# Performance work log

Hardware: AMD Instinct MI355X
Metric: run time of the kernel (lower is better)

## Reference

```python
import jax, jax.numpy as jnp
import numpy as np

N_NODES = 100000
N_EDGES = 1600000
IN_CH = 128
HID = 128
BN_EPS = 1e-5


def setup_inputs() -> dict:
    key = jax.random.key(0)
    ks = jax.random.split(key, 16)
    x = jax.random.normal(ks[0], (N_NODES, IN_CH), dtype=jnp.float32)
    edge_index = jax.random.randint(ks[1], (2, N_EDGES), 0, N_NODES, dtype=jnp.int32)
    edge_attr = jax.random.uniform(ks[2], (N_EDGES,), dtype=jnp.float32)
    def glorot(k, fan_in, fan_out):
        s = jnp.sqrt(6.0 / (fan_in + fan_out))
        return jax.random.uniform(k, (fan_in, fan_out), dtype=jnp.float32, minval=-s, maxval=s)
    W1 = glorot(ks[3], IN_CH, HID)
    b1 = jnp.zeros((HID,), jnp.float32)
    gamma1 = jnp.ones((HID,), jnp.float32)
    beta1 = jnp.zeros((HID,), jnp.float32)
    W2 = glorot(ks[4], HID, HID)
    b2 = jnp.zeros((HID,), jnp.float32)
    gamma2 = jnp.ones((HID,), jnp.float32)
    beta2 = jnp.zeros((HID,), jnp.float32)
    W3 = glorot(ks[5], HID, 1)
    b3 = jnp.zeros((1,), jnp.float32)
    return {"x": x, "edge_index": edge_index, "edge_attr": edge_attr,
            "W1": W1, "b1": b1, "gamma1": gamma1, "beta1": beta1,
            "W2": W2, "b2": b2, "gamma2": gamma2, "beta2": beta2,
            "W3": W3, "b3": b3}


def _gcn_norm(edge_index, edge_weight, num_nodes):
    # PyG gcn_norm with add_self_loops=True, self-loop weight 1.0
    sl = jnp.arange(num_nodes, dtype=edge_index.dtype)
    row = jnp.concatenate([edge_index[0], sl])  # source
    col = jnp.concatenate([edge_index[1], sl])  # target
    w = jnp.concatenate([edge_weight, jnp.ones((num_nodes,), edge_weight.dtype)])
    deg = jax.ops.segment_sum(w, col, num_segments=num_nodes)
    dinv = jnp.where(deg > 0, jax.lax.rsqrt(jnp.maximum(deg, 1e-30)), 0.0)
    norm = dinv[row] * w * dinv[col]
    return row, col, norm


def _gcn_conv(x, W, b, row, col, norm, num_nodes):
    xw = x @ W                       # [N, out]
    msg = xw[row] * norm[:, None]    # gather + scale, [E+N, out]
    out = jax.ops.segment_sum(msg, col, num_segments=num_nodes)  # scatter-add
    return out + b


def _batchnorm(x, gamma, beta):
    mean = jnp.mean(x, axis=0)
    var = jnp.mean(jnp.square(x - mean), axis=0)  # biased var (torch BN)
    return (x - mean) * jax.lax.rsqrt(var + BN_EPS) * gamma + beta


def reference(x, edge_index, edge_attr, W1, b1, gamma1, beta1, W2, b2, gamma2, beta2, W3, b3):
    n = x.shape[0]
    row, col, norm = _gcn_norm(edge_index, edge_attr, n)
    h = _gcn_conv(x, W1, b1, row, col, norm, n)
    h = jax.nn.relu(_batchnorm(h, gamma1, beta1))  # dropout = identity (eval)
    h = _gcn_conv(h, W2, b2, row, col, norm, n)
    h = jax.nn.relu(_batchnorm(h, gamma2, beta2))
    out = _gcn_conv(h, W3, b3, row, col, norm, n)  # [N, 1]
    return out
```

## Files before the change

kernel.cpp:

```cpp
#include <hip/hip_runtime.h>
#include <hip/hip_bf16.h>


#define HID 128
#define BN_EPS 1e-5f
#define BK 48
#define NPB 128
#define NBMAX 1024
#define CH_A 6144
#define BINCAP 2432

typedef __attribute__((ext_vector_type(8))) short bf16x8;
typedef __attribute__((ext_vector_type(4))) float f32x4;

static inline size_t alignup(size_t x){ return (x + 255) & ~(size_t)255; }


static __device__ inline float2 bf16pair(unsigned int u){
  __hip_bfloat162 h = *(__hip_bfloat162*)&u;
  return __bfloat1622float2(h);
}

static __device__ inline unsigned int packpair(float x, float y){
  __hip_bfloat162 p = __float22bfloat162_rn({x, y});
  return *(unsigned int*)&p;
}

static __device__ inline uint2 pack_bf16x4(float4 a){
  uint2 r;
  r.x = packpair(a.x, a.y);
  r.y = packpair(a.z, a.w);
  return r;
}

static __device__ inline unsigned short bfbits(float v){
  __hip_bfloat16 h = __float2bfloat16(v);
  return *(unsigned short*)&h;
}

__global__ void k_wtprep2(const float* __restrict__ W1, const float* __restrict__ W2,
                          unsigned short* __restrict__ wt1, unsigned short* __restrict__ wt2){
  int idx = blockIdx.x*256 + threadIdx.x;
  const float* Wg = (idx < 16384) ? W1 : W2;
  unsigned short* WTg = (idx < 16384) ? wt1 : wt2;
  int i = idx & 16383;
  int k   = i >> 7;
  int col = i & 127;
  WTg[(size_t)col*128 + k] = bfbits(Wg[(size_t)k*128 + col]);
}


__global__ __launch_bounds__(256) void k_partA(const int* __restrict__ ei,
    const float* __restrict__ attr, int* __restrict__ binCur,
    int2* __restrict__ binbuf, int E){
  __shared__ int hist[NBMAX];
  __shared__ int pref[NBMAX];
  __shared__ int gbase[NBMAX];
  __shared__ int tmp[256];
  __shared__ int2 stage[CH_A];
  __shared__ unsigned short sbin[CH_A];
  int e0 = blockIdx.x * CH_A;
  for (int b = threadIdx.x; b < NBMAX; b += 256) hist[b] = 0;
  __syncthreads();
  #pragma unroll
  for (int k = 0; k < CH_A/256; ++k){
    int e = e0 + k*256 + threadIdx.x;
    if (e < E) atomicAdd(&hist[ei[E + e] >> 7], 1);
  }
  __syncthreads();
  int b4 = threadIdx.x * 4;
  int h0 = hist[b4], h1 = hist[b4+1], h2 = hist[b4+2], h3 = hist[b4+3];
  int lsum = h0 + h1 + h2 + h3;
  tmp[threadIdx.x] = lsum;
  __syncthreads();
  #pragma unroll
  for (int d = 1; d < 256; d <<= 1){
    int t = (threadIdx.x >= d) ? tmp[threadIdx.x - d] : 0;
    __syncthreads();
    tmp[threadIdx.x] += t;
    __syncthreads();
  }
  int ex = tmp[threadIdx.x] - lsum;
  pref[b4]   = ex;
  pref[b4+1] = ex + h0;
  pref[b4+2] = ex + h0 + h1;
  pref[b4+3] = ex + h0 + h1 + h2;
  gbase[b4]   = h0 ? atomicAdd(&binCur[b4],   h0) : 0;
  gbase[b4+1] = h1 ? atomicAdd(&binCur[b4+1], h1) : 0;
  gbase[b4+2] = h2 ? atomicAdd(&binCur[b4+2], h2) : 0;
  gbase[b4+3] = h3 ? atomicAdd(&binCur[b4+3], h3) : 0;
  hist[b4] = pref[b4]; hist[b4+1] = pref[b4+1];
  hist[b4+2] = pref[b4+2]; hist[b4+3] = pref[b4+3];
  __syncthreads();
  #pragma unroll
  for (int k = 0; k < CH_A/256; ++k){
    int e = e0 + k*256 + threadIdx.x;
    if (e < E){
      int d = ei[E + e];
      int s = ei[e];
      int bin = d >> 7;
      int p = atomicAdd(&hist[bin], 1);
      stage[p] = make_int2(s | ((d & 127) << 17), __float_as_int(attr[e]));
      sbin[p] = (unsigned short)bin;
    }
  }
  __syncthreads();
  int cnt = (e0 + CH_A <= E) ? CH_A : max(E - e0, 0);
  for (int i = threadIdx.x; i < cnt; i += 256){
    int bin = sbin[i];
    int off = gbase[bin] + (i - pref[bin]);
    if (off < BINCAP)
      binbuf[(size_t)bin*BINCAP + off] = stage[i];
  }
}

__global__ __launch_bounds__(256) void k_partB(const int2* __restrict__ binbuf,
    const int* __restrict__ binCur, int2* __restrict__ csr,
    int* __restrict__ cnt, float* __restrict__ dinv, int N){
  __shared__ int2 lb[NPB*BK];
  __shared__ int lcnt[NPB];
  int bin = blockIdx.x;
  int node0 = bin * NPB;
  for (int i = threadIdx.x; i < NPB; i += 256) lcnt[i] = 0;
  __syncthreads();
  int m = min(binCur[bin], BINCAP);
  for (int i = threadIdx.x; i < m; i += 256){
    int2 rec = binbuf[(size_t)bin*BINCAP + i];
    int dlo = (rec.x >> 17) & 127;
    int s   = rec.x & 0x1FFFF;
    int p = atomicAdd(&lcnt[dlo], 1);
    if (p < BK) lb[dlo*BK + p] = make_int2(s, rec.y);
  }
  __syncthreads();
  if (threadIdx.x < NPB){
    int node = node0 + threadIdx.x;
    if (node < N){
      int c = min(lcnt[threadIdx.x], BK);
      float s = 0.f;
      for (int k = 0; k < c; ++k) s += __int_as_float(lb[threadIdx.x*BK + k].y);
      cnt[node] = c;
      dinv[node] = 1.0f / sqrtf(1.0f + s);
    }
  }
  int lim = min(NPB, N - node0) * BK;
  for (int i = threadIdx.x; i < lim; i += 256)
    csr[(size_t)node0*BK + i] = lb[i];
}

template<bool BN, bool AB16>
__device__ inline void gemm_body(const void* __restrict__ Av,
    const unsigned short* __restrict__ WTg, const float* __restrict__ coef,
    const float* __restrict__ dinv,
    unsigned int* __restrict__ C, int n, int bid){
  int lane = threadIdx.x & 63;
  int wv4  = threadIdx.x >> 6;
  int l16  = lane & 15;
  int kg   = lane >> 4;
  int row_base = bid*128 + wv4*32;
  int nm1 = n - 1;
  int a0row = min(row_base + l16,      nm1);
  int a1row = min(row_base + 16 + l16, nm1);

  f32x4 acc[2][8] = {};
  #pragma unroll
  for (int k0 = 0; k0 < 128; k0 += 32){
    int k = k0 + kg*8;
    float4 sca, scb, sha, shb;
    if (BN){
      sca = *(const float4*)(coef + k);
      scb = *(const float4*)(coef + k + 4);
      sha = *(const float4*)(coef + 128 + k);
      shb = *(const float4*)(coef + 128 + k + 4);
    }
    bf16x8 a0, a1;
    if constexpr (AB16){
      const unsigned int* A = (const unsigned int*)Av;
      uint4 u0 = *(const uint4*)(A + (size_t)a0row*64 + (k >> 1));
      uint4 u1 = *(const uint4*)(A + (size_t)a1row*64 + (k >> 1));
      #pragma unroll
      for (int half = 0; half < 2; ++half){
        uint4 u = half ? u1 : u0;
        float2 p0 = bf16pair(u.x), p1 = bf16pair(u.y);
        float2 p2 = bf16pair(u.z), p3 = bf16pair(u.w);
        if (BN){
          p0.x = fmaxf(fmaf(p0.x, sca.x, sha.x), 0.f);
          p0.y = fmaxf(fmaf(p0.y, sca.y, sha.y), 0.f);
          p1.x = fmaxf(fmaf(p1.x, sca.z, sha.z), 0.f);
          p1.y = fmaxf(fmaf(p1.y, sca.w, sha.w), 0.f);
          p2.x = fmaxf(fmaf(p2.x, scb.x, shb.x), 0.f);
          p2.y = fmaxf(fmaf(p2.y, scb.y, shb.y), 0.f);
          p3.x = fmaxf(fmaf(p3.x, scb.z, shb.z), 0.f);
          p3.y = fmaxf(fmaf(p3.y, scb.w, shb.w), 0.f);
        }
        union { bf16x8 v; unsigned int u[4]; } c;
        c.u[0] = packpair(p0.x, p0.y);
        c.u[1] = packpair(p1.x, p1.y);
        c.u[2] = packpair(p2.x, p2.y);
        c.u[3] = packpair(p3.x, p3.y);
        if (half) a1 = c.v; else a0 = c.v;
      }
    } else {
      const float* A = (const float*)Av;
      float4 lo0 = *(const float4*)(A + (size_t)a0row*HID + k);
      float4 hi0 = *(const float4*)(A + (size_t)a0row*HID + k + 4);
      float4 lo1 = *(const float4*)(A + (size_t)a1row*HID + k);
      float4 hi1 = *(const float4*)(A + (size_t)a1row*HID + k + 4);
      union { bf16x8 v; uint2 u[2]; } a0c, a1c;
      a0c.u[0] = pack_bf16x4(lo0); a0c.u[1] = pack_bf16x4(hi0);
      a1c.u[0] = pack_bf16x4(lo1); a1c.u[1] = pack_bf16x4(hi1);
      a0 = a0c.v; a1 = a1c.v;
    }
    #pragma unroll
    for (int ct = 0; ct < 8; ++ct){
      int col = ct*16 + l16;
      bf16x8 b = *(const bf16x8*)(WTg + (size_t)col*128 + k);
      acc[0][ct] = __builtin_amdgcn_mfma_f32_16x16x32_bf16(a0, b, acc[0][ct], 0,0,0);
      acc[1][ct] = __builtin_amdgcn_mfma_f32_16x16x32_bf16(a1, b, acc[1][ct], 0,0,0);
    }
  }

  #pragma unroll
  for (int rt = 0; rt < 2; ++rt){
    int growb = row_base + rt*16 + kg*4;
    #pragma unroll
    for (int r = 0; r < 4; ++r){
      int grow = growb + r;
      bool ok = (grow < n) && !(lane & 1);
      float dv = ok ? dinv[grow] : 0.f;
      #pragma unroll
      for (int ct = 0; ct < 8; ++ct){
        float v = acc[rt][ct][r];
        float o = __shfl_xor(v, 1);
        if (ok)
          C[(size_t)grow*64 + ct*8 + (l16 >> 1)] = packpair(v*dv, o*dv);
      }
    }
  }
}

__global__ __launch_bounds__(256) void k_gemm_mfma_s(const float* __restrict__ A,
    const unsigned short* __restrict__ WTg, const float* __restrict__ dinv,
    unsigned int* __restrict__ C, int n){
  gemm_body<false,false>(A, WTg, nullptr, dinv, C, n, blockIdx.x);
}

__global__ __launch_bounds__(256) void k_gemm_mfma_bn16_s(const unsigned int* __restrict__ A,
    const unsigned short* __restrict__ WTg, const float* __restrict__ coef,
    const float* __restrict__ dinv, unsigned int* __restrict__ C, int n){
  gemm_body<true,true>(A, WTg, coef, dinv, C, n, blockIdx.x);
}


struct Acc8 { float a0,a1,a2,a3,a4,a5,a6,a7; };

static __device__ inline void fma8(Acc8& a, uint4 v, float wt){
  float2 p0 = bf16pair(v.x), p1 = bf16pair(v.y);
  float2 p2 = bf16pair(v.z), p3 = bf16pair(v.w);
  a.a0 = fmaf(wt, p0.x, a.a0); a.a1 = fmaf(wt, p0.y, a.a1);
  a.a2 = fmaf(wt, p1.x, a.a2); a.a3 = fmaf(wt, p1.y, a.a3);
  a.a4 = fmaf(wt, p2.x, a.a4); a.a5 = fmaf(wt, p2.y, a.a5);
  a.a6 = fmaf(wt, p3.x, a.a6); a.a7 = fmaf(wt, p3.y, a.a7);
}

__global__ __launch_bounds__(256) void k_gather128(const unsigned int* __restrict__ yb,
    const int2* __restrict__ csr, const int* __restrict__ cnt,
    const float* __restrict__ dinv, const float* __restrict__ bias,
    unsigned int* __restrict__ out, int n){
  int node = blockIdx.x*4 + (threadIdx.x >> 6);
  int lane = threadIdx.x & 63;
  if (node >= n) return;
  int l16 = lane & 15;
  int eg  = lane >> 4;
  size_t base = (size_t)node*BK;
  int m = min(cnt[node], BK);
  Acc8 a = {0,0,0,0,0,0,0,0};
  float di = 0.f;
  float4 b0 = {0,0,0,0}, b1 = {0,0,0,0};
  if (eg == 0){
    di = dinv[node];
    uint4 sv = *(const uint4*)(yb + (size_t)node*64 + l16*4);
    b0 = *(const float4*)(bias + l16*8);
    b1 = *(const float4*)(bias + l16*8 + 4);
    float2 p0 = bf16pair(sv.x), p1 = bf16pair(sv.y);
    float2 p2 = bf16pair(sv.z), p3 = bf16pair(sv.w);
    a.a0 = p0.x; a.a1 = p0.y; a.a2 = p1.x; a.a3 = p1.y;
    a.a4 = p2.x; a.a5 = p2.y; a.a6 = p3.x; a.a7 = p3.y;
  }
  int j = eg;
  for (; j + 12 < m; j += 16){
    int2 e0 = csr[base + j];
    int2 e1 = csr[base + j + 4];
    int2 e2 = csr[base + j + 8];
    int2 e3 = csr[base + j + 12];
    uint4 v0 = *(const uint4*)(yb + (size_t)e0.x*64 + l16*4);
    uint4 v1 = *(const uint4*)(yb + (size_t)e1.x*64 + l16*4);
    uint4 v2 = *(const uint4*)(yb + (size_t)e2.x*64 + l16*4);
    uint4 v3 = *(const uint4*)(yb + (size_t)e3.x*64 + l16*4);
    fma8(a, v0, __int_as_float(e0.y));
    fma8(a, v1, __int_as_float(e1.y));
    fma8(a, v2, __int_as_float(e2.y));
    fma8(a, v3, __int_as_float(e3.y));
  }
  for (; j < m; j += 4){
    int2 ea = csr[base + j];
    uint4 va = *(const uint4*)(yb + (size_t)ea.x*64 + l16*4);
    fma8(a, va, __int_as_float(ea.y));
  }
  a.a0 += __shfl_xor(a.a0, 16); a.a1 += __shfl_xor(a.a1, 16);
  a.a2 += __shfl_xor(a.a2, 16); a.a3 += __shfl_xor(a.a3, 16);
  a.a4 += __shfl_xor(a.a4, 16); a.a5 += __shfl_xor(a.a5, 16);
  a.a6 += __shfl_xor(a.a6, 16); a.a7 += __shfl_xor(a.a7, 16);
  a.a0 += __shfl_xor(a.a0, 32); a.a1 += __shfl_xor(a.a1, 32);
  a.a2 += __shfl_xor(a.a2, 32); a.a3 += __shfl_xor(a.a3, 32);
  a.a4 += __shfl_xor(a.a4, 32); a.a5 += __shfl_xor(a.a5, 32);
  a.a6 += __shfl_xor(a.a6, 32); a.a7 += __shfl_xor(a.a7, 32);
  if (eg == 0){
    uint4 r;
    r.x = packpair(fmaf(di, a.a0, b0.x), fmaf(di, a.a1, b0.y));
    r.y = packpair(fmaf(di, a.a2, b0.z), fmaf(di, a.a3, b0.w));
    r.z = packpair(fmaf(di, a.a4, b1.x), fmaf(di, a.a5, b1.y));
    r.w = packpair(fmaf(di, a.a6, b1.z), fmaf(di, a.a7, b1.w));
    *(uint4*)(out + (size_t)node*64 + l16*4) = r;
  }
}

__global__ __launch_bounds__(256) void k_bnstats(const unsigned int* __restrict__ h,
                                                 float* stats, int n){
  __shared__ float ls0[256], ls1[256], lq0[256], lq1[256];
  int p  = threadIdx.x & 63;
  int r0 = blockIdx.x*4 + (threadIdx.x >> 6);
  float s0=0.f, s1=0.f, q0=0.f, q1=0.f;
  for (int r = r0; r < n; r += gridDim.x*4){
    float2 v = bf16pair(h[(size_t)r*64 + p]);
    s0 += v.x; q0 = fmaf(v.x, v.x, q0);
    s1 += v.y; q1 = fmaf(v.y, v.y, q1);
  }
  ls0[threadIdx.x]=s0; ls1[threadIdx.x]=s1; lq0[threadIdx.x]=q0; lq1[threadIdx.x]=q1;
  __syncthreads();
  if (threadIdx.x < 64){
    int t = threadIdx.x;
    s0 = ls0[t]+ls0[t+64]+ls0[t+128]+ls0[t+192];
    s1 = ls1[t]+ls1[t+64]+ls1[t+128]+ls1[t+192];
    q0 = lq0[t]+lq0[t+64]+lq0[t+128]+lq0[t+192];
    q1 = lq1[t]+lq1[t+64]+lq1[t+128]+lq1[t+192];
    atomicAdd(&stats[2*t],       s0);
    atomicAdd(&stats[2*t+1],     s1);
    atomicAdd(&stats[128+2*t],   q0);
    atomicAdd(&stats[128+2*t+1], q1);
  }
}

__global__ void k_bnfin(const float* __restrict__ stats, const float* __restrict__ gamma,
                        const float* __restrict__ beta, float* coef, int n){
  int c = threadIdx.x;
  float inv_n = 1.0f / (float)n;
  float mean = stats[c] * inv_n;
  float var = fmaxf(stats[128 + c] * inv_n - mean*mean, 0.f);
  float sc = gamma[c] / sqrtf(var + BN_EPS);
  coef[c] = sc;
  coef[128 + c] = fmaf(-mean, sc, beta[c]);
}

__global__ __launch_bounds__(256) void k_dotW3(const unsigned int* __restrict__ h,
    const float* __restrict__ coef, const float* __restrict__ W3,
    const float* __restrict__ dinv, float* __restrict__ y3, int n){
  int lane = threadIdx.x & 31;
  int row = blockIdx.x*8 + (threadIdx.x >> 5);
  if (row >= n) return;
  uint2 u = *(const uint2*)(h + (size_t)row*64 + lane*2);
  float2 va = bf16pair(u.x), vb = bf16pair(u.y);
  float4 sc = *(const float4*)(coef + lane*4);
  float4 sh = *(const float4*)(coef + 128 + lane*4);
  float4 w  = *(const float4*)(W3 + lane*4);
  float acc = fmaxf(fmaf(va.x, sc.x, sh.x), 0.f) * w.x
            + fmaxf(fmaf(va.y, sc.y, sh.y), 0.f) * w.y
            + fmaxf(fmaf(vb.x, sc.z, sh.z), 0.f) * w.z
            + fmaxf(fmaf(vb.y, sc.w, sh.w), 0.f) * w.w;
  #pragma unroll
  for (int mm = 1; mm < 32; mm <<= 1) acc += __shfl_xor(acc, mm, 32);
  if (lane == 0) y3[row] = acc * dinv[row];
}

__global__ void k_gather1(const float* __restrict__ y3, const int2* __restrict__ csr,
    const int* __restrict__ cnt, const float* __restrict__ dinv,
    const float* __restrict__ b3, float* __restrict__ out, int n){
  int i = blockIdx.x*256 + threadIdx.x;
  if (i >= n) return;
  float acc = y3[i];
  size_t base = (size_t)i*BK;
  int m = min(cnt[i], BK);
  for (int j = 0; j < m; ++j){
    int2 e = csr[base + j];
    acc = fmaf(__int_as_float(e.y), y3[e.x], acc);
  }
  out[i] = fmaf(dinv[i], acc, b3[0]);
}

extern "C" void kernel_launch(void* const* d_in, const int* in_sizes, int n_in,
                              void* d_out, int out_size, void* d_ws, size_t ws_size,
                              hipStream_t stream){
  const float* x    = (const float*)d_in[0];
  const int*   ei   = (const int*)  d_in[1];
  const float* attr = (const float*)d_in[2];
  const float* W1   = (const float*)d_in[3];
  const float* b1   = (const float*)d_in[4];
  const float* g1   = (const float*)d_in[5];
  const float* be1  = (const float*)d_in[6];
  const float* W2   = (const float*)d_in[7];
  const float* b2   = (const float*)d_in[8];
  const float* g2   = (const float*)d_in[9];
  const float* be2  = (const float*)d_in[10];
  const float* W3   = (const float*)d_in[11];
  const float* b3   = (const float*)d_in[12];
  float* out = (float*)d_out;

  const int N = in_sizes[0] / HID;
  const int E = in_sizes[2];
  const int nbins = (N + NPB - 1) / NPB;

  char* w = (char*)d_ws;
  auto take = [&](size_t bytes) -> char* { char* p = w; w += alignup(bytes); return p; };
  int*   binCur = (int*)  take((size_t)NBMAX*4);
  int*   cnt    = (int*)  take((size_t)N*4);
  float* dinv   = (float*)take((size_t)N*4);
  float* stats  = (float*)take(256*4);
  float* coef1  = (float*)take(256*4);
  float* coef2  = (float*)take(256*4);
  unsigned short* wt1 = (unsigned short*)take(128*128*2);
  unsigned short* wt2 = (unsigned short*)take(128*128*2);
  int2*  binbuf = (int2*) take((size_t)nbins*BINCAP*8);
  int2*  csr    = (int2*) take((size_t)N*BK*8);
  float* y3     = (float*)take((size_t)N*4);
  unsigned int* bufA = (unsigned int*)take((size_t)N*64*4);
  unsigned int* bufB = (unsigned int*)take((size_t)N*64*4);
  (void)ws_size; (void)n_in; (void)out_size;

  int nbN = (N + 255)/256;
  int nbA = (E + CH_A - 1)/CH_A;
  int nbG = (N + 127)/128;

  hipMemsetAsync(binCur, 0, (size_t)NBMAX*4, stream);
  k_wtprep2  <<<128,   256, 0, stream>>>(W1, W2, wt1, wt2);
  k_partA    <<<nbA,   256, 0, stream>>>(ei, attr, binCur, binbuf, E);
  k_partB    <<<nbins, 256, 0, stream>>>(binbuf, binCur, csr, cnt, dinv, N);
  k_gemm_mfma_s<<<nbG, 256, 0, stream>>>(x, wt1, dinv, bufA, N);

  k_gather128<<<(N+3)/4, 256, 0, stream>>>(bufA, csr, cnt, dinv, b1, bufB, N);
  hipMemsetAsync(stats, 0, 256*4, stream);
  k_bnstats  <<<512, 256, 0, stream>>>(bufB, stats, N);
  k_bnfin    <<<1, 128, 0, stream>>>(stats, g1, be1, coef1, N);

  k_gemm_mfma_bn16_s<<<nbG, 256, 0, stream>>>(bufB, wt2, coef1, dinv, bufA, N);
  k_gather128<<<(N+3)/4, 256, 0, stream>>>(bufA, csr, cnt, dinv, b2, bufB, N);
  hipMemsetAsync(stats, 0, 256*4, stream);
  k_bnstats  <<<512, 256, 0, stream>>>(bufB, stats, N);
  k_bnfin    <<<1, 128, 0, stream>>>(stats, g2, be2, coef2, N);

  k_dotW3    <<<(N+7)/8, 256, 0, stream>>>(bufB, coef2, W3, dinv, y3, N);
  k_gather1  <<<nbN, 256, 0, stream>>>(y3, csr, cnt, dinv, b3, out, N);
}
```

Before: 399.5 us.

## Shard hidden features into 16-column slabs and gather per shard

Changes the hidden feature buffers from row-major [N,128] bf16 to eight column shards of [N,16], each 32 bytes per node. GEMM writes and reads, BN stats and the W3 dot product are updated to match. The gather kernel now launches eight blocks per node group, one per shard, so each wave reads 32-byte rows of a 3.2 MB shard that is more likely to stay in cache. Each wave also reads the CSR list eight times (once per shard), using nontemporal loads, and issues many small 4-byte gathers instead of 16-byte ones.

Result: slower. 899.6 us (+125.2%).

```diff
diff --git a/kernel.cpp b/kernel.cpp
--- a/kernel.cpp
+++ b/kernel.cpp
@@ -160,6 +160,7 @@
   int nm1 = n - 1;
   int a0row = min(row_base + l16,      nm1);
   int a1row = min(row_base + 16 + l16, nm1);
+  size_t shstride = (size_t)n * 8;
 
   f32x4 acc[2][8] = {};
   #pragma unroll
@@ -175,8 +176,9 @@
     bf16x8 a0, a1;
     if constexpr (AB16){
       const unsigned int* A = (const unsigned int*)Av;
-      uint4 u0 = *(const uint4*)(A + (size_t)a0row*64 + (k >> 1));
-      uint4 u1 = *(const uint4*)(A + (size_t)a1row*64 + (k >> 1));
+      size_t abase = (size_t)(k >> 4) * shstride + ((k >> 3) & 1) * 4;
+      uint4 u0 = *(const uint4*)(A + abase + (size_t)a0row*8);
+      uint4 u1 = *(const uint4*)(A + abase + (size_t)a1row*8);
       #pragma unroll
       for (int half = 0; half < 2; ++half){
         uint4 u = half ? u1 : u0;
@@ -232,7 +234,7 @@
         float v = acc[rt][ct][r];
         float o = __shfl_xor(v, 1);
         if (ok)
-          C[(size_t)grow*64 + ct*8 + (l16 >> 1)] = packpair(v*dv, o*dv);
+          C[(size_t)ct*shstride + (size_t)grow*8 + (l16 >> 1)] = packpair(v*dv, o*dv);
       }
     }
   }
@@ -250,88 +252,60 @@
   gemm_body<true,true>(A, WTg, coef, dinv, C, n, blockIdx.x);
 }
 
-
-struct Acc8 { float a0,a1,a2,a3,a4,a5,a6,a7; };
-
-static __device__ inline void fma8(Acc8& a, uint4 v, float wt){
-  float2 p0 = bf16pair(v.x), p1 = bf16pair(v.y);
-  float2 p2 = bf16pair(v.z), p3 = bf16pair(v.w);
-  a.a0 = fmaf(wt, p0.x, a.a0); a.a1 = fmaf(wt, p0.y, a.a1);
-  a.a2 = fmaf(wt, p1.x, a.a2); a.a3 = fmaf(wt, p1.y, a.a3);
-  a.a4 = fmaf(wt, p2.x, a.a4); a.a5 = fmaf(wt, p2.y, a.a5);
-  a.a6 = fmaf(wt, p3.x, a.a6); a.a7 = fmaf(wt, p3.y, a.a7);
-}
-
-__global__ __launch_bounds__(256) void k_gather128(const unsigned int* __restrict__ yb,
+__global__ __launch_bounds__(256) void k_gatherS(const unsigned int* __restrict__ yb,
     const int2* __restrict__ csr, const int* __restrict__ cnt,
     const float* __restrict__ dinv, const float* __restrict__ bias,
-    unsigned int* __restrict__ out, int n){
-  int node = blockIdx.x*4 + (threadIdx.x >> 6);
+    unsigned int* __restrict__ out, int N){
+  int shard = blockIdx.x & 7;
+  int node = (blockIdx.x >> 3)*4 + (threadIdx.x >> 6);
+  if (node >= N) return;
   int lane = threadIdx.x & 63;
-  if (node >= n) return;
-  int l16 = lane & 15;
-  int eg  = lane >> 4;
-  size_t base = (size_t)node*BK;
+  int g  = lane >> 3;
+  int cl = lane & 7;
+  const unsigned int* ys = yb + (size_t)shard * N * 8;
+  size_t base = (size_t)node * BK;
   int m = min(cnt[node], BK);
-  Acc8 a = {0,0,0,0,0,0,0,0};
-  float di = 0.f;
-  float4 b0 = {0,0,0,0}, b1 = {0,0,0,0};
-  if (eg == 0){
-    di = dinv[node];
-    uint4 sv = *(const uint4*)(yb + (size_t)node*64 + l16*4);
-    b0 = *(const float4*)(bias + l16*8);
-    b1 = *(const float4*)(bias + l16*8 + 4);
-    float2 p0 = bf16pair(sv.x), p1 = bf16pair(sv.y);
-    float2 p2 = bf16pair(sv.z), p3 = bf16pair(sv.w);
-    a.a0 = p0.x; a.a1 = p0.y; a.a2 = p1.x; a.a3 = p1.y;
-    a.a4 = p2.x; a.a5 = p2.y; a.a6 = p3.x; a.a7 = p3.y;
-  }
-  int j = eg;
-  for (; j + 12 < m; j += 16){
-    int2 e0 = csr[base + j];
-    int2 e1 = csr[base + j + 4];
-    int2 e2 = csr[base + j + 8];
-    int2 e3 = csr[base + j + 12];
-    uint4 v0 = *(const uint4*)(yb + (size_t)e0.x*64 + l16*4);
-    uint4 v1 = *(const uint4*)(yb + (size_t)e1.x*64 + l16*4);
-    uint4 v2 = *(const uint4*)(yb + (size_t)e2.x*64 + l16*4);
-    uint4 v3 = *(const uint4*)(yb + (size_t)e3.x*64 + l16*4);
-    fma8(a, v0, __int_as_float(e0.y));
-    fma8(a, v1, __int_as_float(e1.y));
-    fma8(a, v2, __int_as_float(e2.y));
-    fma8(a, v3, __int_as_float(e3.y));
-  }
-  for (; j < m; j += 4){
-    int2 ea = csr[base + j];
-    uint4 va = *(const uint4*)(yb + (size_t)ea.x*64 + l16*4);
-    fma8(a, va, __int_as_float(ea.y));
-  }
-  a.a0 += __shfl_xor(a.a0, 16); a.a1 += __shfl_xor(a.a1, 16);
-  a.a2 += __shfl_xor(a.a2, 16); a.a3 += __shfl_xor(a.a3, 16);
-  a.a4 += __shfl_xor(a.a4, 16); a.a5 += __shfl_xor(a.a5, 16);
-  a.a6 += __shfl_xor(a.a6, 16); a.a7 += __shfl_xor(a.a7, 16);
-  a.a0 += __shfl_xor(a.a0, 32); a.a1 += __shfl_xor(a.a1, 32);
-  a.a2 += __shfl_xor(a.a2, 32); a.a3 += __shfl_xor(a.a3, 32);
-  a.a4 += __shfl_xor(a.a4, 32); a.a5 += __shfl_xor(a.a5, 32);
-  a.a6 += __shfl_xor(a.a6, 32); a.a7 += __shfl_xor(a.a7, 32);
-  if (eg == 0){
-    uint4 r;
-    r.x = packpair(fmaf(di, a.a0, b0.x), fmaf(di, a.a1, b0.y));
-    r.y = packpair(fmaf(di, a.a2, b0.z), fmaf(di, a.a3, b0.w));
-    r.z = packpair(fmaf(di, a.a4, b1.x), fmaf(di, a.a5, b1.y));
-    r.w = packpair(fmaf(di, a.a6, b1.z), fmaf(di, a.a7, b1.w));
-    *(uint4*)(out + (size_t)node*64 + l16*4) = r;
-  }
-}
+  float a0 = 0.f, a1 = 0.f;
+  int j = g;
+  for (; j + 8 < m; j += 16){
+    long long p0 = __builtin_nontemporal_load((const long long*)&csr[base + j]);
+    long long p1 = __builtin_nontemporal_load((const long long*)&csr[base + j + 8]);
+    int s0 = (int)(p0 & 0xffffffffLL); float w0 = __int_as_float((int)(p0 >> 32));
+    int s1 = (int)(p1 & 0xffffffffLL); float w1 = __int_as_float((int)(p1 >> 32));
+    unsigned int u0 = ys[(size_t)s0*8 + cl];
+    unsigned int u1 = ys[(size_t)s1*8 + cl];
+    float2 v0 = bf16pair(u0), v1 = bf16pair(u1);
+    a0 = fmaf(w0, v0.x, a0); a1 = fmaf(w0, v0.y, a1);
+    a0 = fmaf(w1, v1.x, a0); a1 = fmaf(w1, v1.y, a1);
+  }
+  if (j < m){
+    long long p0 = __builtin_nontemporal_load((const long long*)&csr[base + j]);
+    int s0 = (int)(p0 & 0xffffffffLL); float w0 = __int_as_float((int)(p0 >> 32));
+    float2 v0 = bf16pair(ys[(size_t)s0*8 + cl]);
+    a0 = fmaf(w0, v0.x, a0); a1 = fmaf(w0, v0.y, a1);
+  }
+  a0 += __shfl_xor(a0, 8);  a1 += __shfl_xor(a1, 8);
+  a0 += __shfl_xor(a0, 16); a1 += __shfl_xor(a1, 16);
+  a0 += __shfl_xor(a0, 32); a1 += __shfl_xor(a1, 32);
+  if (g == 0){
+    float di = dinv[node];
+    float2 sv = bf16pair(ys[(size_t)node*8 + cl]);
+    float2 bv = *(const float2*)(bias + shard*16 + cl*2);
+    unsigned int r = packpair(fmaf(di, a0 + sv.x, bv.x), fmaf(di, a1 + sv.y, bv.y));
+    __builtin_nontemporal_store(r, &out[(size_t)shard*N*8 + (size_t)node*8 + cl]);
+  }
+}
+
 
 __global__ __launch_bounds__(256) void k_bnstats(const unsigned int* __restrict__ h,
                                                  float* stats, int n){
   __shared__ float ls0[256], ls1[256], lq0[256], lq1[256];
   int p  = threadIdx.x & 63;
+  size_t hbase = (size_t)(p >> 3) * n * 8 + (p & 7);
   int r0 = blockIdx.x*4 + (threadIdx.x >> 6);
   float s0=0.f, s1=0.f, q0=0.f, q1=0.f;
   for (int r = r0; r < n; r += gridDim.x*4){
-    float2 v = bf16pair(h[(size_t)r*64 + p]);
+    float2 v = bf16pair(h[hbase + (size_t)r*8]);
     s0 += v.x; q0 = fmaf(v.x, v.x, q0);
     s1 += v.y; q1 = fmaf(v.y, v.y, q1);
   }
@@ -367,7 +341,7 @@
   int lane = threadIdx.x & 31;
   int row = blockIdx.x*8 + (threadIdx.x >> 5);
   if (row >= n) return;
-  uint2 u = *(const uint2*)(h + (size_t)row*64 + lane*2);
+  uint2 u = *(const uint2*)(h + (size_t)(lane >> 2)*n*8 + (size_t)row*8 + (lane & 3)*2);
   float2 va = bf16pair(u.x), vb = bf16pair(u.y);
   float4 sc = *(const float4*)(coef + lane*4);
   float4 sh = *(const float4*)(coef + 128 + lane*4);
@@ -438,6 +412,7 @@
   int nbN = (N + 255)/256;
   int nbA = (E + CH_A - 1)/CH_A;
   int nbG = (N + 127)/128;
+  int nbS = ((N + 3)/4) * 8;
 
   hipMemsetAsync(binCur, 0, (size_t)NBMAX*4, stream);
   k_wtprep2  <<<128,   256, 0, stream>>>(W1, W2, wt1, wt2);
@@ -445,13 +420,13 @@
   k_partB    <<<nbins, 256, 0, stream>>>(binbuf, binCur, csr, cnt, dinv, N);
   k_gemm_mfma_s<<<nbG, 256, 0, stream>>>(x, wt1, dinv, bufA, N);
 
-  k_gather128<<<(N+3)/4, 256, 0, stream>>>(bufA, csr, cnt, dinv, b1, bufB, N);
+  k_gatherS  <<<nbS, 256, 0, stream>>>(bufA, csr, cnt, dinv, b1, bufB, N);
   hipMemsetAsync(stats, 0, 256*4, stream);
   k_bnstats  <<<512, 256, 0, stream>>>(bufB, stats, N);
   k_bnfin    <<<1, 128, 0, stream>>>(stats, g1, be1, coef1, N);
 
   k_gemm_mfma_bn16_s<<<nbG, 256, 0, stream>>>(bufB, wt2, coef1, dinv, bufA, N);
-  k_gather128<<<(N+3)/4, 256, 0, stream>>>(bufA, csr, cnt, dinv, b2, bufB, N);
+  k_gatherS  <<<nbS, 256, 0, stream>>>(bufA, csr, cnt, dinv, b2, bufB, N);
   hipMemsetAsync(stats, 0, 256*4, stream);
   k_bnstats  <<<512, 256, 0, stream>>>(bufB, stats, N);
   k_bnfin    <<<1, 128, 0, stream>>>(stats, g2, be2, coef2, N);
```
